# Performance work log

Measured on AMD Instinct MI355X. Metric: run time of the kernel, lower is better.

The kernel has to match this reference:

```python
import jax, jax.numpy as jnp
import numpy as np

# Hard-coded backbone constants from the original module
N_INIT = np.array([17.047, 14.099, 3.625], dtype=np.float32)
CA_INIT = np.array([16.967, 12.784, 4.338], dtype=np.float32)
C_INIT = np.array([15.685, 12.755, 5.133], dtype=np.float32)
LEN_C_N, LEN_N_CA, LEN_CA_C = 1.34, 1.46, 1.54
ANG_C_N = 115.0 / 180.0 * np.pi
ANG_N_CA = 121.0 / 180.0 * np.pi
ANG_CA_C = 109.0 / 180.0 * np.pi


def _unit(x):
    return x / jnp.linalg.norm(x, axis=-1, keepdims=True)


def _place_dihedral(a, b, c, bond_angle, bond_length, torsion):
    # a,b,c: [B,3]; torsion: [B]; bond_angle/bond_length: python floats
    ab = b - a
    bc = _unit(c - b)
    n = _unit(jnp.cross(ab, bc))
    nbc = jnp.cross(n, bc)
    d0 = -bond_length * jnp.cos(bond_angle)              # scalar
    d1 = bond_length * jnp.cos(torsion) * jnp.sin(bond_angle)  # [B]
    d2 = bond_length * jnp.sin(torsion) * jnp.sin(bond_angle)  # [B]
    # d = m^T @ [d0,d1,d2] with m rows = (bc, nbc, n)
    return c + d0 * bc + d1[:, None] * nbc + d2[:, None] * n


def setup_inputs() -> dict:
    key = jax.random.key(0)
    k1, k2, k3 = jax.random.split(key, 3)
    B, L = 4096, 512
    return {
        "phi": jax.random.normal(k1, (B, L), dtype=jnp.float32),
        "psi": jax.random.normal(k2, (B, L), dtype=jnp.float32),
        "omega": jax.random.normal(k3, (B, L), dtype=jnp.float32),
        "max_length": 512,
    }


def reference(phi, psi, omega, max_length):
    B, L = phi.shape
    steps = min(L - 1, max_length - 1)
    # initial N, CA, C coords repeated over batch: each [B,3]
    a0 = jnp.broadcast_to(jnp.asarray(N_INIT), (B, 3))
    b0 = jnp.broadcast_to(jnp.asarray(CA_INIT), (B, 3))
    c0 = jnp.broadcast_to(jnp.asarray(C_INIT), (B, 3))

    # per-step torsions: psi_i, omega_i, phi_{i+1}
    xs = (psi[:, :steps].T, omega[:, :steps].T, phi[:, 1:steps + 1].T)  # each [steps,B]

    def step(carry, tors):
        a, b, c = carry
        t_psi, t_omega, t_phi = tors
        d_n = _place_dihedral(a, b, c, ANG_C_N, LEN_C_N, t_psi)
        d_ca = _place_dihedral(b, c, d_n, ANG_N_CA, LEN_N_CA, t_omega)
        d_c = _place_dihedral(c, d_n, d_ca, ANG_CA_C, LEN_CA_C, t_phi)
        return (d_n, d_ca, d_c), jnp.stack([d_n, d_ca, d_c], axis=0)

    _, ys = jax.lax.scan(step, (a0, b0, c0), xs)  # ys: [steps,3,B,3]
    new_coords = jnp.transpose(ys, (2, 0, 1, 3)).reshape(B, 3 * steps, 3)
    init = jnp.stack([a0, b0, c0], axis=1)  # [B,3,3]
    return jnp.concatenate([init, new_coords], axis=1)  # [B, 3*(steps+1), 3]
```

## Files before the change

### kernel.cpp

```cpp
#include <hip/hip_runtime.h>


struct V3 { float x, y, z; };

__device__ __forceinline__ V3 vsub(V3 a, V3 b){ return {a.x-b.x, a.y-b.y, a.z-b.z}; }
__device__ __forceinline__ V3 vcross(V3 a, V3 b){
    return {a.y*b.z - a.z*b.y, a.z*b.x - a.x*b.z, a.x*b.y - a.y*b.x};
}
__device__ __forceinline__ float vdot(V3 a, V3 b){ return a.x*b.x + a.y*b.y + a.z*b.z; }
__device__ __forceinline__ V3 vunit(V3 a){
    float r = rsqrtf(vdot(a,a));
    return {a.x*r, a.y*r, a.z*r};
}

struct Xform { V3 c0, c1, c2, t; };

__device__ __forceinline__ V3 xrot(const Xform& X, V3 p){
    return { X.c0.x*p.x + X.c1.x*p.y + X.c2.x*p.z,
             X.c0.y*p.x + X.c1.y*p.y + X.c2.y*p.z,
             X.c0.z*p.x + X.c1.z*p.y + X.c2.z*p.z };
}
__device__ __forceinline__ V3 xapply(const Xform& X, V3 p){
    V3 r = xrot(X, p);
    return { r.x + X.t.x, r.y + X.t.y, r.z + X.t.z };
}
__device__ __forceinline__ Xform xcompose(const Xform& A, const Xform& B){
    Xform R;
    R.c0 = xrot(A, B.c0);
    R.c1 = xrot(A, B.c1);
    R.c2 = xrot(A, B.c2);
    R.t  = xapply(A, B.t);
    return R;
}

__device__ __forceinline__ Xform frame_of(V3 A, V3 B, V3 C){
    V3 bc  = vunit(vsub(C, B));
    V3 n   = vunit(vcross(vsub(B, A), bc));
    V3 nbc = vcross(n, bc);
    return { bc, nbc, n, C };
}

__device__ __forceinline__ Xform shfl_up_xf(const Xform& X, int d){
    Xform R;
    R.c0.x = __shfl_up(X.c0.x, d); R.c0.y = __shfl_up(X.c0.y, d); R.c0.z = __shfl_up(X.c0.z, d);
    R.c1.x = __shfl_up(X.c1.x, d); R.c1.y = __shfl_up(X.c1.y, d); R.c1.z = __shfl_up(X.c1.z, d);
    R.c2.x = __shfl_up(X.c2.x, d); R.c2.y = __shfl_up(X.c2.y, d); R.c2.z = __shfl_up(X.c2.z, d);
    R.t.x  = __shfl_up(X.t.x,  d); R.t.y  = __shfl_up(X.t.y,  d); R.t.z  = __shfl_up(X.t.z,  d);
    return R;
}

#define D0_CN   0.56630847f
#define LS_CN   1.21445243f
#define D0_NCA  0.75195559f
#define LS_NCA  1.25146426f
#define D0_CAC  0.50137496f
#define LS_CAC  1.45609861f

#define A0X (-2.0153295f)
#define A0Y ( 1.3804571f)

#define NIX 17.047f
#define NIY 14.099f
#define NIZ  3.625f
#define CAX 16.967f
#define CAY 12.784f
#define CAZ  4.338f
#define CIX 15.685f
#define CIY 12.755f
#define CIZ  5.133f

__device__ __forceinline__ V3 place_dihedral(V3 a, V3 b, V3 c,
                                             float d0, float Ls, float tor){
    V3 ab = vsub(b, a);
    V3 bc = vunit(vsub(c, b));
    V3 n  = vunit(vcross(ab, bc));
    V3 nbc = vcross(n, bc);
    float sn, cs;
    __sincosf(tor, &sn, &cs);
    float d1 = Ls * cs;
    float d2 = Ls * sn;
    return { c.x + d0*bc.x + d1*nbc.x + d2*n.x,
             c.y + d0*bc.y + d1*nbc.y + d2*n.y,
             c.z + d0*bc.z + d1*nbc.z + d2*n.z };
}

__device__ __forceinline__ void step3(V3& A, V3& B, V3& C,
                                      float tpsi, float tome, float tphi){
    V3 dn  = place_dihedral(A, B, C,  D0_CN,  LS_CN,  tpsi);
    V3 dca = place_dihedral(B, C, dn, D0_NCA, LS_NCA, tome);
    V3 dc  = place_dihedral(C, dn, dca, D0_CAC, LS_CAC, tphi);
    A = dn; B = dca; C = dc;
}

__device__ __forceinline__ void put4(float4* lds4, int p, float4 v){
    lds4[p ^ ((p >> 6) & 7)] = v;
}

__device__ __forceinline__ void stage36(float4* lds4, int p,
    V3 aA, V3 aB, V3 aC, V3 bA, V3 bB, V3 bC,
    V3 cA, V3 cB, V3 cC, V3 dA, V3 dB, V3 dC){
    put4(lds4, p+0, make_float4(aA.x, aA.y, aA.z, aB.x));
    put4(lds4, p+1, make_float4(aB.y, aB.z, aC.x, aC.y));
    put4(lds4, p+2, make_float4(aC.z, bA.x, bA.y, bA.z));
    put4(lds4, p+3, make_float4(bB.x, bB.y, bB.z, bC.x));
    put4(lds4, p+4, make_float4(bC.y, bC.z, cA.x, cA.y));
    put4(lds4, p+5, make_float4(cA.z, cB.x, cB.y, cB.z));
    put4(lds4, p+6, make_float4(cC.x, cC.y, cC.z, dA.x));
    put4(lds4, p+7, make_float4(dA.y, dA.z, dB.x, dB.y));
    put4(lds4, p+8, make_float4(dB.z, dC.x, dC.y, dC.z));
}

__global__ __launch_bounds__(64, 3)
void nerf_half(const float* __restrict__ phi,
               const float* __restrict__ psi,
               const float* __restrict__ omega,
               float* __restrict__ out,
               int steps){
    const int L = 512;
    int b = blockIdx.x;
    int k = threadIdx.x;
    int s0 = k * 8;

    __shared__ float4 lds4[576];

    const float* pphi = phi   + (size_t)b * L;
    const float* ppsi = psi   + (size_t)b * L;
    const float* pome = omega + (size_t)b * L;

    float4 ps0 = ((const float4*)(ppsi + s0))[0];
    float4 ps1 = ((const float4*)(ppsi + s0))[1];
    float4 om0 = ((const float4*)(pome + s0))[0];
    float4 om1 = ((const float4*)(pome + s0))[1];
    float4 ph0 = ((const float4*)(pphi + s0))[0];
    float4 ph1 = ((const float4*)(pphi + s0))[1];
    float phi8 = __shfl_down(ph0.x, 1);

    float tpsi[8] = {ps0.x, ps0.y, ps0.z, ps0.w, ps1.x, ps1.y, ps1.z, ps1.w};
    float tome[8] = {om0.x, om0.y, om0.z, om0.w, om1.x, om1.y, om1.z, om1.w};
    float tphi[8] = {ph0.y, ph0.z, ph0.w, ph1.x, ph1.y, ph1.z, ph1.w, phi8};

    V3 A, Bv, C;
    if (k == 0){
        A = {NIX, NIY, NIZ}; Bv = {CAX, CAY, CAZ}; C = {CIX, CIY, CIZ};
    } else {
        A = {A0X, A0Y, 0.f}; Bv = {-1.54f, 0.f, 0.f}; C = {0.f, 0.f, 0.f};
    }
    V3 locA[8], locB[8], locC[8];
    #pragma unroll
    for (int s = 0; s < 8; ++s){
        if (s0 + s < steps)
            step3(A, Bv, C, tpsi[s], tome[s], tphi[s]);
        locA[s] = A; locB[s] = Bv; locC[s] = C;
    }
    Xform V = frame_of(A, Bv, C);

    #pragma unroll
    for (int d = 1; d < 64; d <<= 1){
        Xform Pr = shfl_up_xf(V, d);
        if (k >= d) V = xcompose(Pr, V);
    }
    Xform Wp = shfl_up_xf(V, 1);

    if (k != 0){
        #pragma unroll
        for (int s = 0; s < 8; ++s){
            locA[s] = xapply(Wp, locA[s]);
            locB[s] = xapply(Wp, locB[s]);
            locC[s] = xapply(Wp, locC[s]);
        }
    }

    V3 nA, nB, nC;
    nA.x = __shfl_up(locA[7].x, 1); nA.y = __shfl_up(locA[7].y, 1); nA.z = __shfl_up(locA[7].z, 1);
    nB.x = __shfl_up(locB[7].x, 1); nB.y = __shfl_up(locB[7].y, 1); nB.z = __shfl_up(locB[7].z, 1);
    nC.x = __shfl_up(locC[7].x, 1); nC.y = __shfl_up(locC[7].y, 1); nC.z = __shfl_up(locC[7].z, 1);
    if (k == 0){
        nA = {NIX, NIY, NIZ}; nB = {CAX, CAY, CAZ}; nC = {CIX, CIY, CIZ};
    }

    int m = k & 31;
    int p0 = 18 * m;
    float4* o4 = (float4*)(out + (size_t)b * 4608u);

    if (k < 32){
        stage36(lds4, p0,     nA, nB, nC, locA[0], locB[0], locC[0],
                              locA[1], locB[1], locC[1], locA[2], locB[2], locC[2]);
        stage36(lds4, p0 + 9, locA[3], locB[3], locC[3], locA[4], locB[4], locC[4],
                              locA[5], locB[5], locC[5], locA[6], locB[6], locC[6]);
    }
    __syncthreads();
    #pragma unroll
    for (int i = 0; i < 9; ++i){
        int q = i * 64 + k;
        o4[q] = lds4[q ^ ((q >> 6) & 7)];
    }
    __syncthreads();

    if (k >= 32){
        stage36(lds4, p0,     nA, nB, nC, locA[0], locB[0], locC[0],
                              locA[1], locB[1], locC[1], locA[2], locB[2], locC[2]);
        stage36(lds4, p0 + 9, locA[3], locB[3], locC[3], locA[4], locB[4], locC[4],
                              locA[5], locB[5], locC[5], locA[6], locB[6], locC[6]);
    }
    __syncthreads();
    #pragma unroll
    for (int i = 0; i < 9; ++i){
        int q = i * 64 + k;
        o4[576 + q] = lds4[q ^ ((q >> 6) & 7)];
    }
}

__global__ void nerf_seq_kernel(const float* __restrict__ phi,
                                const float* __restrict__ psi,
                                const float* __restrict__ omega,
                                float* __restrict__ out,
                                int B, int L, int steps){
    int b = blockIdx.x * blockDim.x + threadIdx.x;
    if (b >= B) return;
    V3 A  = {NIX, NIY, NIZ};
    V3 Bv = {CAX, CAY, CAZ};
    V3 C  = {CIX, CIY, CIZ};
    float* o = out + (size_t)b * 9u * (size_t)(steps + 1);
    o[0]=A.x;  o[1]=A.y;  o[2]=A.z;
    o[3]=Bv.x; o[4]=Bv.y; o[5]=Bv.z;
    o[6]=C.x;  o[7]=C.y;  o[8]=C.z;
    const float* pphi = phi   + (size_t)b * L;
    const float* ppsi = psi   + (size_t)b * L;
    const float* pome = omega + (size_t)b * L;
    for (int s = 0; s < steps; ++s){
        step3(A, Bv, C, ppsi[s], pome[s], pphi[s + 1]);
        float* os = o + 9u * (size_t)(s + 1);
        os[0]=A.x;  os[1]=A.y;  os[2]=A.z;
        os[3]=Bv.x; os[4]=Bv.y; os[5]=Bv.z;
        os[6]=C.x;  os[7]=C.y;  os[8]=C.z;
    }
}

extern "C" void kernel_launch(void* const* d_in, const int* in_sizes, int n_in,
                              void* d_out, int out_size, void* d_ws, size_t ws_size,
                              hipStream_t stream) {
    const float* phi   = (const float*)d_in[0];
    const float* psi   = (const float*)d_in[1];
    const float* omega = (const float*)d_in[2];
    float* out = (float*)d_out;

    const int L = 512;
    int B = in_sizes[0] / L;
    int steps = out_size / (9 * B) - 1;

    if (steps == 511 && in_sizes[0] == B * 512) {
        nerf_half<<<B, 64, 0, stream>>>(phi, psi, omega, out, steps);
    } else {
        int block = 64;
        int grid = (B + block - 1) / block;
        nerf_seq_kernel<<<grid, block, 0, stream>>>(phi, psi, omega, out, B, L, steps);
    }
}
```

Before: 30.98 us.

## Split each chain into two independent halves per lane with dual prefix scans

Each lane now computes two 4-step segments (one in each half of the 512-residue chain) instead of one 8-step segment, giving two independent dependency chains per thread for ILP. Two wave-wide transform scans run interleaved, and the second half is rebased by the broadcast final transform of the first half. This shortens the serial per-lane chain and lets both halves write out with all 64 lanes staging each pass, at the cost of more shuffles and an extra compose plus more live registers.

```diff
diff --git a/kernel.cpp b/kernel.cpp
--- a/kernel.cpp
+++ b/kernel.cpp
@@ -46,6 +46,14 @@
     R.c1.x = __shfl_up(X.c1.x, d); R.c1.y = __shfl_up(X.c1.y, d); R.c1.z = __shfl_up(X.c1.z, d);
     R.c2.x = __shfl_up(X.c2.x, d); R.c2.y = __shfl_up(X.c2.y, d); R.c2.z = __shfl_up(X.c2.z, d);
     R.t.x  = __shfl_up(X.t.x,  d); R.t.y  = __shfl_up(X.t.y,  d); R.t.z  = __shfl_up(X.t.z,  d);
+    return R;
+}
+__device__ __forceinline__ Xform shfl_bc_xf(const Xform& X, int lane){
+    Xform R;
+    R.c0.x = __shfl(X.c0.x, lane); R.c0.y = __shfl(X.c0.y, lane); R.c0.z = __shfl(X.c0.z, lane);
+    R.c1.x = __shfl(X.c1.x, lane); R.c1.y = __shfl(X.c1.y, lane); R.c1.z = __shfl(X.c1.z, lane);
+    R.c2.x = __shfl(X.c2.x, lane); R.c2.y = __shfl(X.c2.y, lane); R.c2.z = __shfl(X.c2.z, lane);
+    R.t.x  = __shfl(X.t.x,  lane); R.t.y  = __shfl(X.t.y,  lane); R.t.z  = __shfl(X.t.z,  lane);
     return R;
 }
 
@@ -111,7 +119,7 @@
 }
 
 __global__ __launch_bounds__(64, 3)
-void nerf_half(const float* __restrict__ phi,
+void nerf_dual(const float* __restrict__ phi,
                const float* __restrict__ psi,
                const float* __restrict__ omega,
                float* __restrict__ out,
@@ -119,7 +127,8 @@
     const int L = 512;
     int b = blockIdx.x;
     int k = threadIdx.x;
-    int s0 = k * 8;
+    int sA = 4 * k;
+    int sB = 256 + 4 * k;
 
     __shared__ float4 lds4[576];
 
@@ -127,67 +136,91 @@
     const float* ppsi = psi   + (size_t)b * L;
     const float* pome = omega + (size_t)b * L;
 
-    float4 ps0 = ((const float4*)(ppsi + s0))[0];
-    float4 ps1 = ((const float4*)(ppsi + s0))[1];
-    float4 om0 = ((const float4*)(pome + s0))[0];
-    float4 om1 = ((const float4*)(pome + s0))[1];
-    float4 ph0 = ((const float4*)(pphi + s0))[0];
-    float4 ph1 = ((const float4*)(pphi + s0))[1];
-    float phi8 = __shfl_down(ph0.x, 1);
-
-    float tpsi[8] = {ps0.x, ps0.y, ps0.z, ps0.w, ps1.x, ps1.y, ps1.z, ps1.w};
-    float tome[8] = {om0.x, om0.y, om0.z, om0.w, om1.x, om1.y, om1.z, om1.w};
-    float tphi[8] = {ph0.y, ph0.z, ph0.w, ph1.x, ph1.y, ph1.z, ph1.w, phi8};
-
-    V3 A, Bv, C;
+    float4 psA = *(const float4*)(ppsi + sA);
+    float4 psB = *(const float4*)(ppsi + sB);
+    float4 omA = *(const float4*)(pome + sA);
+    float4 omB = *(const float4*)(pome + sB);
+    float4 phA = *(const float4*)(pphi + sA);
+    float4 phB = *(const float4*)(pphi + sB);
+    float phnA  = __shfl_down(phA.x, 1);
+    float ph256 = __shfl(phB.x, 0);
+    if (k == 63) phnA = ph256;
+    float phnB  = __shfl_down(phB.x, 1);
+
+    float tpsiA[4] = {psA.x, psA.y, psA.z, psA.w};
+    float tomeA[4] = {omA.x, omA.y, omA.z, omA.w};
+    float tphiA[4] = {phA.y, phA.z, phA.w, phnA};
+    float tpsiB[4] = {psB.x, psB.y, psB.z, psB.w};
+    float tomeB[4] = {omB.x, omB.y, omB.z, omB.w};
+    float tphiB[4] = {phB.y, phB.z, phB.w, phnB};
+
+    V3 Aa, Ba, Ca, Ab, Bb, Cb;
     if (k == 0){
-        A = {NIX, NIY, NIZ}; Bv = {CAX, CAY, CAZ}; C = {CIX, CIY, CIZ};
+        Aa = {NIX, NIY, NIZ}; Ba = {CAX, CAY, CAZ}; Ca = {CIX, CIY, CIZ};
     } else {
-        A = {A0X, A0Y, 0.f}; Bv = {-1.54f, 0.f, 0.f}; C = {0.f, 0.f, 0.f};
-    }
-    V3 locA[8], locB[8], locC[8];
-    #pragma unroll
-    for (int s = 0; s < 8; ++s){
-        if (s0 + s < steps)
-            step3(A, Bv, C, tpsi[s], tome[s], tphi[s]);
-        locA[s] = A; locB[s] = Bv; locC[s] = C;
-    }
-    Xform V = frame_of(A, Bv, C);
+        Aa = {A0X, A0Y, 0.f}; Ba = {-1.54f, 0.f, 0.f}; Ca = {0.f, 0.f, 0.f};
+    }
+    Ab = {A0X, A0Y, 0.f}; Bb = {-1.54f, 0.f, 0.f}; Cb = {0.f, 0.f, 0.f};
+
+    V3 lAa[4], lBa[4], lCa[4], lAb[4], lBb[4], lCb[4];
+    #pragma unroll
+    for (int s = 0; s < 4; ++s){
+        step3(Aa, Ba, Ca, tpsiA[s], tomeA[s], tphiA[s]);
+        if (sB + s < steps)
+            step3(Ab, Bb, Cb, tpsiB[s], tomeB[s], tphiB[s]);
+        lAa[s] = Aa; lBa[s] = Ba; lCa[s] = Ca;
+        lAb[s] = Ab; lBb[s] = Bb; lCb[s] = Cb;
+    }
+    Xform Va = frame_of(Aa, Ba, Ca);
+    Xform Vb = frame_of(Ab, Bb, Cb);
 
     #pragma unroll
     for (int d = 1; d < 64; d <<= 1){
-        Xform Pr = shfl_up_xf(V, d);
-        if (k >= d) V = xcompose(Pr, V);
-    }
-    Xform Wp = shfl_up_xf(V, 1);
+        Xform Pa = shfl_up_xf(Va, d);
+        Xform Pb = shfl_up_xf(Vb, d);
+        if (k >= d){ Va = xcompose(Pa, Va); Vb = xcompose(Pb, Vb); }
+    }
+    Xform T1  = shfl_bc_xf(Va, 63);
+    Xform Wpa = shfl_up_xf(Va, 1);
+    Xform Upb = shfl_up_xf(Vb, 1);
 
     if (k != 0){
         #pragma unroll
-        for (int s = 0; s < 8; ++s){
-            locA[s] = xapply(Wp, locA[s]);
-            locB[s] = xapply(Wp, locB[s]);
-            locC[s] = xapply(Wp, locC[s]);
+        for (int s = 0; s < 4; ++s){
+            lAa[s] = xapply(Wpa, lAa[s]);
+            lBa[s] = xapply(Wpa, lBa[s]);
+            lCa[s] = xapply(Wpa, lCa[s]);
         }
     }
-
-    V3 nA, nB, nC;
-    nA.x = __shfl_up(locA[7].x, 1); nA.y = __shfl_up(locA[7].y, 1); nA.z = __shfl_up(locA[7].z, 1);
-    nB.x = __shfl_up(locB[7].x, 1); nB.y = __shfl_up(locB[7].y, 1); nB.z = __shfl_up(locB[7].z, 1);
-    nC.x = __shfl_up(locC[7].x, 1); nC.y = __shfl_up(locC[7].y, 1); nC.z = __shfl_up(locC[7].z, 1);
+    Xform Wpb = (k == 0) ? T1 : xcompose(T1, Upb);
+    #pragma unroll
+    for (int s = 0; s < 4; ++s){
+        lAb[s] = xapply(Wpb, lAb[s]);
+        lBb[s] = xapply(Wpb, lBb[s]);
+        lCb[s] = xapply(Wpb, lCb[s]);
+    }
+
+    V3 nAa, nBa, nCa;
+    nAa.x = __shfl_up(lAa[3].x, 1); nAa.y = __shfl_up(lAa[3].y, 1); nAa.z = __shfl_up(lAa[3].z, 1);
+    nBa.x = __shfl_up(lBa[3].x, 1); nBa.y = __shfl_up(lBa[3].y, 1); nBa.z = __shfl_up(lBa[3].z, 1);
+    nCa.x = __shfl_up(lCa[3].x, 1); nCa.y = __shfl_up(lCa[3].y, 1); nCa.z = __shfl_up(lCa[3].z, 1);
+    float bAx = __shfl(lAa[3].x, 63), bAy = __shfl(lAa[3].y, 63), bAz = __shfl(lAa[3].z, 63);
+    float bBx = __shfl(lBa[3].x, 63), bBy = __shfl(lBa[3].y, 63), bBz = __shfl(lBa[3].z, 63);
+    float bCx = __shfl(lCa[3].x, 63), bCy = __shfl(lCa[3].y, 63), bCz = __shfl(lCa[3].z, 63);
+    V3 nAb, nBb, nCb;
+    nAb.x = __shfl_up(lAb[3].x, 1); nAb.y = __shfl_up(lAb[3].y, 1); nAb.z = __shfl_up(lAb[3].z, 1);
+    nBb.x = __shfl_up(lBb[3].x, 1); nBb.y = __shfl_up(lBb[3].y, 1); nBb.z = __shfl_up(lBb[3].z, 1);
+    nCb.x = __shfl_up(lCb[3].x, 1); nCb.y = __shfl_up(lCb[3].y, 1); nCb.z = __shfl_up(lCb[3].z, 1);
     if (k == 0){
-        nA = {NIX, NIY, NIZ}; nB = {CAX, CAY, CAZ}; nC = {CIX, CIY, CIZ};
-    }
-
-    int m = k & 31;
-    int p0 = 18 * m;
+        nAa = {NIX, NIY, NIZ}; nBa = {CAX, CAY, CAZ}; nCa = {CIX, CIY, CIZ};
+        nAb = {bAx, bAy, bAz}; nBb = {bBx, bBy, bBz}; nCb = {bCx, bCy, bCz};
+    }
+
+    int p0 = 9 * k;
     float4* o4 = (float4*)(out + (size_t)b * 4608u);
 
-    if (k < 32){
-        stage36(lds4, p0,     nA, nB, nC, locA[0], locB[0], locC[0],
-                              locA[1], locB[1], locC[1], locA[2], locB[2], locC[2]);
-        stage36(lds4, p0 + 9, locA[3], locB[3], locC[3], locA[4], locB[4], locC[4],
-                              locA[5], locB[5], locC[5], locA[6], locB[6], locC[6]);
-    }
+    stage36(lds4, p0, nAa, nBa, nCa, lAa[0], lBa[0], lCa[0],
+                      lAa[1], lBa[1], lCa[1], lAa[2], lBa[2], lCa[2]);
     __syncthreads();
     #pragma unroll
     for (int i = 0; i < 9; ++i){
@@ -196,12 +229,8 @@
     }
     __syncthreads();
 
-    if (k >= 32){
-        stage36(lds4, p0,     nA, nB, nC, locA[0], locB[0], locC[0],
-                              locA[1], locB[1], locC[1], locA[2], locB[2], locC[2]);
-        stage36(lds4, p0 + 9, locA[3], locB[3], locC[3], locA[4], locB[4], locC[4],
-                              locA[5], locB[5], locC[5], locA[6], locB[6], locC[6]);
-    }
+    stage36(lds4, p0, nAb, nBb, nCb, lAb[0], lBb[0], lCb[0],
+                      lAb[1], lBb[1], lCb[1], lAb[2], lBb[2], lCb[2]);
     __syncthreads();
     #pragma unroll
     for (int i = 0; i < 9; ++i){
@@ -249,7 +278,7 @@
     int steps = out_size / (9 * B) - 1;
 
     if (steps == 511 && in_sizes[0] == B * 512) {
-        nerf_half<<<B, 64, 0, stream>>>(phi, psi, omega, out, steps);
+        nerf_dual<<<B, 64, 0, stream>>>(phi, psi, omega, out, steps);
     } else {
         int block = 64;
         int grid = (B + block - 1) / block;
```

Measured after the change: 36.17 us. 1.17x slower.
